# Kernel tuning notes

Hardware: AMD Instinct MI355X
Metric: run time of the kernel (lower is better)

Reference implementation:

```python
import jax, jax.numpy as jnp
import numpy as np
from jax import lax

N = 8192          # number of proposals
CLASSES = 81      # includes background class 0
PAD = 300         # padding (max detections kept)
NMS_THRESH = 0.5


def _decode_and_pick(metadata, deltas, proposals, scores):
    """bbox_transform_inv + clip + per-row argmax class gather (keras_rcnn math)."""
    scale = metadata[0, 2]
    boxes = proposals.reshape(-1, 4) / scale                      # (N,4) x1,y1,x2,y2
    n = boxes.shape[0]
    d = deltas.reshape(n, -1, 4)                                  # (N,C,4) dx,dy,dw,dh
    s = scores.reshape(n, -1)                                     # (N,C)

    w = boxes[:, 2] - boxes[:, 0] + 1.0
    h = boxes[:, 3] - boxes[:, 1] + 1.0
    cx = boxes[:, 0] + 0.5 * w
    cy = boxes[:, 1] + 0.5 * h

    pcx = d[:, :, 0] * w[:, None] + cx[:, None]
    pcy = d[:, :, 1] * h[:, None] + cy[:, None]
    pw = jnp.exp(d[:, :, 2]) * w[:, None]
    ph = jnp.exp(d[:, :, 3]) * h[:, None]

    pred = jnp.stack([pcx - 0.5 * pw, pcy - 0.5 * ph,
                      pcx + 0.5 * pw, pcy + 0.5 * ph], axis=-1)   # (N,C,4)

    # clip to image: x cols to [0, W-1], y cols to [0, H-1]; metadata[0,:2]=(H,W)
    H, W = metadata[0, 0], metadata[0, 1]
    lim = jnp.stack([W - 1.0, H - 1.0, W - 1.0, H - 1.0])
    pred = jnp.clip(pred, 0.0, lim)

    top = jnp.argmax(s, axis=1)                                   # (N,)
    sel = jnp.take_along_axis(pred, top[:, None, None], axis=1)[:, 0, :]  # (N,4)
    max_scores = jnp.max(s[:, 1:], axis=1)                        # exclude background
    return sel, s, max_scores


def _nms_indices(boxes, scores):
    """Greedy NMS; returns (PAD,) kept indices + float validity mask."""
    n = boxes.shape[0]
    order = jnp.argsort(-scores)
    b = boxes[order]
    x1, y1, x2, y2 = b[:, 0], b[:, 1], b[:, 2], b[:, 3]
    area = jnp.maximum(x2 - x1, 0.0) * jnp.maximum(y2 - y1, 0.0)
    lt = jnp.maximum(b[:, None, :2], b[None, :, :2])
    rb = jnp.minimum(b[:, None, 2:], b[None, :, 2:])
    wh = jnp.maximum(rb - lt, 0.0)
    inter = wh[..., 0] * wh[..., 1]                               # (N,N)
    iou = inter / (area[:, None] + area[None, :] - inter + 1e-8)

    idx = jnp.arange(n)

    def step(suppressed, xs):
        iou_row, i = xs
        keep_i = jnp.logical_not(suppressed[i])
        suppressed = suppressed | (keep_i & (iou_row > NMS_THRESH) & (idx > i))
        return suppressed, keep_i

    _, keep = lax.scan(step, jnp.zeros((n,), bool), (iou, idx))    # keep in sorted order

    rank = jnp.cumsum(keep.astype(jnp.int32)) - 1
    pos = jnp.where(keep & (rank < PAD), rank, PAD)               # overflow slot PAD
    buf = jnp.zeros((PAD + 1,), jnp.int32).at[pos].set(order.astype(jnp.int32))
    keep_idx = buf[:PAD]
    num_kept = jnp.minimum(jnp.sum(keep.astype(jnp.int32)), PAD)
    valid = (jnp.arange(PAD) < num_kept).astype(boxes.dtype)
    return keep_idx, valid


def setup_inputs() -> dict:
    key = jax.random.key(0)
    k1, k2, k3, k4, k5, k6 = jax.random.split(key, 6)
    Himg, Wimg, scale = 800.0, 1333.0, 1.5
    metadata = jnp.array([[Himg, Wimg, scale]], dtype=jnp.float32)
    cx = jax.random.uniform(k1, (1, N), minval=0.0, maxval=Wimg * scale)
    cy = jax.random.uniform(k2, (1, N), minval=0.0, maxval=Himg * scale)
    w = jax.random.uniform(k3, (1, N), minval=16.0, maxval=256.0)
    h = jax.random.uniform(k4, (1, N), minval=16.0, maxval=256.0)
    proposals = jnp.stack([cx - 0.5 * w, cy - 0.5 * h,
                           cx + 0.5 * w, cy + 0.5 * h], axis=-1)  # (1,N,4)
    deltas = 0.1 * jax.random.normal(k5, (1, N, 4 * CLASSES), dtype=jnp.float32)
    scores = jax.random.uniform(k6, (1, N, CLASSES), dtype=jnp.float32)
    return {"metadata": metadata, "deltas": deltas,
            "proposals": proposals, "scores": scores}


def reference(metadata, deltas, proposals, scores):
    sel, s, max_scores = _decode_and_pick(metadata, deltas, proposals, scores)
    keep_idx, valid = _nms_indices(lax.stop_gradient(sel),
                                   lax.stop_gradient(max_scores))
    boxes_out = sel[keep_idx] * valid[:, None]                    # (PAD,4), zero-padded
    scores_out = s[keep_idx] * valid[:, None]                     # (PAD,C)
    return boxes_out[None], scores_out[None]
```

## Files before the change

kernel.cpp:

```cpp
#include <hip/hip_runtime.h>

#define N 8192
#define NCLS 81
#define PAD 300
#define NPANEL 16
#define PANW 512

typedef unsigned long long u64;

__device__ __forceinline__ void gload_lds16(const void* g, void* l) {
  __builtin_amdgcn_global_load_lds(
      (const __attribute__((address_space(1))) unsigned int*)g,
      (__attribute__((address_space(3))) unsigned int*)l, 16, 0, 0);
}

__device__ __forceinline__ u64 readlane64(u64 v, int l) {
  unsigned lo = __builtin_amdgcn_readlane((unsigned)v, l);
  unsigned hi = __builtin_amdgcn_readlane((unsigned)(v >> 32), l);
  return ((u64)hi << 32) | lo;
}

__global__ __launch_bounds__(256) void decode_kernel(
    const float* __restrict__ meta, const float* __restrict__ deltas,
    const float* __restrict__ proposals, const float* __restrict__ scores,
    float4* __restrict__ sel, u64* __restrict__ keys, int* __restrict__ rank,
    int* __restrict__ ctr) {
  int tid = threadIdx.x;
  if (blockIdx.x == 0 && tid < 16) ctr[tid] = 0;
  int row = blockIdx.x * 32 + (tid >> 3);
  int sub = tid & 7;
  const float* srow = scores + (size_t)row * NCLS;
  float bs = -1e30f, ms = -1e30f;
  int best = 0;
  for (int c = sub; c < NCLS; c += 8) {
    float v = srow[c];
    if (v > bs) { bs = v; best = c; }
    if (c > 0) ms = fmaxf(ms, v);
  }
#pragma unroll
  for (int d = 1; d < 8; d <<= 1) {
    float ob = __shfl_xor(bs, d);
    int oi = __shfl_xor(best, d);
    float om = __shfl_xor(ms, d);
    if (ob > bs || (ob == bs && oi < best)) { bs = ob; best = oi; }
    ms = fmaxf(ms, om);
  }
  if (sub == 0) {
    float W = meta[1], sc = meta[2], H = meta[0];
    const float* p = proposals + row * 4;
    float x1 = p[0] / sc, y1 = p[1] / sc, x2 = p[2] / sc, y2 = p[3] / sc;
    float w = x2 - x1 + 1.0f, h = y2 - y1 + 1.0f;
    float cx = x1 + 0.5f * w, cy = y1 + 0.5f * h;
    float4 d4 = *(const float4*)(deltas + (size_t)row * (4 * NCLS) + best * 4);
    float pcx = d4.x * w + cx, pcy = d4.y * h + cy;
    float pw = expf(d4.z) * w, ph = expf(d4.w) * h;
    float lx = W - 1.0f, ly = H - 1.0f;
    float ox1 = fminf(fmaxf(pcx - 0.5f * pw, 0.0f), lx);
    float oy1 = fminf(fmaxf(pcy - 0.5f * ph, 0.0f), ly);
    float ox2 = fminf(fmaxf(pcx + 0.5f * pw, 0.0f), lx);
    float oy2 = fminf(fmaxf(pcy + 0.5f * ph, 0.0f), ly);
    sel[row] = make_float4(ox1, oy1, ox2, oy2);
    keys[row] = ((u64)(~__float_as_uint(ms)) << 32) | (unsigned)row;
    rank[row] = 0;
  }
}

__global__ __launch_bounds__(256) void rank_kernel(
    const u64* __restrict__ keys, int* __restrict__ rank) {
  __shared__ u64 kt[256];
  int tid = threadIdx.x;
  int i = blockIdx.x * 256 + tid;
  kt[tid] = keys[blockIdx.y * 256 + tid];
  u64 ki = keys[i];
  __syncthreads();
  int c = 0;
#pragma unroll 8
  for (int t = 0; t < 256; ++t) c += (kt[t] < ki);
  atomicAdd(&rank[i], c);
}

__global__ __launch_bounds__(256) void scatter_kernel(
    const int* __restrict__ rank, const float4* __restrict__ sel,
    int* __restrict__ sortedIdx, float4* __restrict__ sortedBoxes,
    float* __restrict__ sortedArea) {
  int i = blockIdx.x * 256 + threadIdx.x;
  int r = rank[i];
  float4 b = sel[i];
  sortedIdx[r] = i;
  sortedBoxes[r] = b;
  sortedArea[r] = fmaxf(b.z - b.x, 0.0f) * fmaxf(b.w - b.y, 0.0f);
}

__global__ __launch_bounds__(256) void mask_scan_kernel(
    const float4* __restrict__ sboxes, const float* __restrict__ sarea,
    u64* __restrict__ mask, int* __restrict__ kept, int* __restrict__ num_kept,
    int* __restrict__ ctr) {
  __shared__ union {
    u64 slab[PANW * 8];
    struct { float4 cbox[256]; float carea[256]; } m;
  } sh;
  __shared__ int keptGi[PAD];
  int tid = threadIdx.x;

  if (blockIdx.x > 0) {
    int idx = (int)blockIdx.x - 1;
    int cb = idx >> 5, rg = idx & 31;
    if (4 * rg > cb) return;
    int rbase = rg * 256;
    sh.m.cbox[tid] = sboxes[rbase + tid];
    sh.m.carea[tid] = sarea[rbase + tid];
    int lane = tid & 63, wid = tid >> 6;
    float4 bj = sboxes[cb * 64 + lane];
    float aB = sarea[cb * 64 + lane];
    __syncthreads();
    int rlim = cb * 64 + 64;
    int r0 = rbase + (wid << 6);
#pragma unroll 4
    for (int i = 0; i < 32; ++i) {
      int r1 = r0 + i, r2 = r0 + i + 32;
      if (r1 >= rlim) break;
      float4 bi1 = sh.m.cbox[(wid << 6) + i];
      float aA1 = sh.m.carea[(wid << 6) + i];
      float4 bi2 = sh.m.cbox[(wid << 6) + i + 32];
      float aA2 = sh.m.carea[(wid << 6) + i + 32];
      float lx1 = fmaxf(bi1.x, bj.x), ly1 = fmaxf(bi1.y, bj.y);
      float rx1 = fminf(bi1.z, bj.z), ry1 = fminf(bi1.w, bj.w);
      float in1 = fmaxf(rx1 - lx1, 0.0f) * fmaxf(ry1 - ly1, 0.0f);
      float u1 = aA1 + aB - in1 + 1e-8f;
      u64 bits1 = __ballot(((in1 * 33554432.0f - u1 * 16777216.0f) - u1) > 0.0f);
      float lx2 = fmaxf(bi2.x, bj.x), ly2 = fmaxf(bi2.y, bj.y);
      float rx2 = fminf(bi2.z, bj.z), ry2 = fminf(bi2.w, bj.w);
      float in2 = fmaxf(rx2 - lx2, 0.0f) * fmaxf(ry2 - ly2, 0.0f);
      float u2 = aA2 + aB - in2 + 1e-8f;
      u64 bits2 = __ballot(((in2 * 33554432.0f - u2 * 16777216.0f) - u2) > 0.0f);
      if ((r1 >> 6) == cb) bits1 &= ~((2ull << (r1 & 63)) - 1ull);
      if ((r2 >> 6) == cb) bits2 &= ~((2ull << (r2 & 63)) - 1ull);
      if (lane == 0) {
        __hip_atomic_store(&mask[(size_t)r1 * 128 + cb], bits1,
                           __ATOMIC_RELAXED, __HIP_MEMORY_SCOPE_AGENT);
        if (r2 < rlim)
          __hip_atomic_store(&mask[(size_t)r2 * 128 + cb], bits2,
                             __ATOMIC_RELAXED, __HIP_MEMORY_SCOPE_AGENT);
      }
    }
    __syncthreads();
    if (tid == 0)
      __hip_atomic_fetch_add(&ctr[cb >> 3], 1, __ATOMIC_RELEASE,
                             __HIP_MEMORY_SCOPE_AGENT);
    return;
  }

  if (tid >= 64) return;
  int lane = tid;
  int cnt = 0;
  const char* mb = (const char*)mask;

  for (int p = 0; p < NPANEL; ++p) {
    int base = p * PANW;
    int need = 16 * p + 12;
    while (__hip_atomic_load(&ctr[p], __ATOMIC_RELAXED,
                             __HIP_MEMORY_SCOPE_AGENT) < need)
      __builtin_amdgcn_s_sleep(8);
    (void)__hip_atomic_load(&ctr[p], __ATOMIC_ACQUIRE,
                            __HIP_MEMORY_SCOPE_AGENT);

    {
      const char* srcB = mb + (size_t)base * 1024 + (size_t)p * 64;
#pragma unroll
      for (int it = 0; it < 32; ++it) {
        const char* g = srcB + (size_t)(it * 16 + (lane >> 2)) * 1024 + (lane & 3) * 16;
        gload_lds16(g, &sh.slab[0] + it * 128);
      }
    }
    u64 d0 = mask[(size_t)(base + 0 + lane) * 128 + p * 8 + 0];
    u64 d1 = mask[(size_t)(base + 64 + lane) * 128 + p * 8 + 1];
    u64 d2 = mask[(size_t)(base + 128 + lane) * 128 + p * 8 + 2];
    u64 d3 = mask[(size_t)(base + 192 + lane) * 128 + p * 8 + 3];
    u64 d4 = mask[(size_t)(base + 256 + lane) * 128 + p * 8 + 4];
    u64 d5 = mask[(size_t)(base + 320 + lane) * 128 + p * 8 + 5];
    u64 d6 = mask[(size_t)(base + 384 + lane) * 128 + p * 8 + 6];
    u64 d7 = mask[(size_t)(base + 448 + lane) * 128 + p * 8 + 7];
    u64 acc = 0ull;
    for (int k = (lane >> 3); k < cnt; k += 8)
      acc |= mask[(size_t)keptGi[k] * 128 + p * 8 + (lane & 7)];

    asm volatile("s_waitcnt vmcnt(0)" ::: "memory");
    __builtin_amdgcn_sched_barrier(0);

    acc |= __shfl_xor(acc, 8);
    acc |= __shfl_xor(acc, 16);
    acc |= __shfl_xor(acc, 32);
    u64 remv = acc;
    const u64* sl = sh.slab;

    unsigned wm = (unsigned)__ballot(~remv != 0ull) & 0xFFu;
    while (cnt < PAD && wm) {
      int w = __ffs(wm) - 1;
      u64 diagW = (w == 0) ? d0 : (w == 1) ? d1 : (w == 2) ? d2 : (w == 3) ? d3
                : (w == 4) ? d4 : (w == 5) ? d5 : (w == 6) ? d6 : d7;
      u64 cur = __shfl(remv, w);
      u64 kb = 0ull;
      while (true) {
        u64 inv = ~cur;
        if (inv == 0ull) break;
        int b = __ffsll(inv) - 1;
        u64 mrow = readlane64(diagW, b);
        if (lane == 0) kept[cnt] = base + (w << 6) + b;
        keptGi[cnt] = base + (w << 6) + b;
        cnt++;
        kb |= 1ull << b;
        cur |= mrow | (1ull << b);
        if (cnt >= PAD) break;
      }
      u64 t = kb;
      while (t) {
        int b = __ffsll(t) - 1;
        t &= t - 1;
        remv |= sl[((w << 6) + b) * 8 + (lane & 7)];
      }
      if ((lane & 7) == w) remv |= kb;
      if (cnt >= PAD) break;
      wm = (unsigned)__ballot(~remv != 0ull) & 0xFFu;
    }
    if (cnt >= PAD) break;
  }
  asm volatile("s_waitcnt vmcnt(0)" ::: "memory");
  if (lane == 0) *num_kept = cnt;
}

__global__ __launch_bounds__(128) void gather_kernel(
    const int* __restrict__ kept, const int* __restrict__ num_kept_p,
    const int* __restrict__ sortedIdx, const float4* __restrict__ sortedBoxes,
    const float* __restrict__ scores, float* __restrict__ out) {
  int r = blockIdx.x;
  int t = threadIdx.x;
  float* boxes_out = out;
  float* scores_out = out + PAD * 4;
  int nk = *num_kept_p;
  bool valid = r < nk;
  int pos = valid ? kept[r] : 0;
  if (t < NCLS) {
    int orig = sortedIdx[pos];
    scores_out[(size_t)r * NCLS + t] = valid ? scores[(size_t)orig * NCLS + t] : 0.0f;
  }
  if (t == 96) {
    float4 b = sortedBoxes[pos];
    if (!valid) b = make_float4(0.f, 0.f, 0.f, 0.f);
    ((float4*)boxes_out)[r] = b;
  }
}

extern "C" void kernel_launch(void* const* d_in, const int* in_sizes, int n_in,
                              void* d_out, int out_size, void* d_ws, size_t ws_size,
                              hipStream_t stream) {
  const float* meta = (const float*)d_in[0];
  const float* deltas = (const float*)d_in[1];
  const float* proposals = (const float*)d_in[2];
  const float* scores = (const float*)d_in[3];
  float* out = (float*)d_out;
  char* ws = (char*)d_ws;

  float4* sel = (float4*)(ws + 0);
  u64* keys = (u64*)(ws + 131072);
  int* rank = (int*)(ws + 196608);
  int* sortedIdx = (int*)(ws + 229376);
  float4* sortedBoxes = (float4*)(ws + 262144);
  float* sortedArea = (float*)(ws + 393216);
  int* kept = (int*)(ws + 425984);
  int* num_kept = (int*)(ws + 428032);
  int* ctr = (int*)(ws + 428096);
  u64* mask = (u64*)(ws + 458752);

  decode_kernel<<<N / 32, 256, 0, stream>>>(meta, deltas, proposals, scores, sel, keys, rank, ctr);
  rank_kernel<<<dim3(N / 256, N / 256), 256, 0, stream>>>(keys, rank);
  scatter_kernel<<<N / 256, 256, 0, stream>>>(rank, sel, sortedIdx, sortedBoxes, sortedArea);
  mask_scan_kernel<<<1 + 128 * 32, 256, 0, stream>>>(sortedBoxes, sortedArea, mask, kept, num_kept, ctr);
  gather_kernel<<<PAD, 128, 0, stream>>>(kept, num_kept, sortedIdx, sortedBoxes, scores, out);
}
```

Measured before the change: 88.70 us.

## Double-buffer NMS mask slabs with a producer wave prefetching panels

```diff
diff --git a/kernel.cpp b/kernel.cpp
--- a/kernel.cpp
+++ b/kernel.cpp
@@ -96,10 +96,12 @@
     u64* __restrict__ mask, int* __restrict__ kept, int* __restrict__ num_kept,
     int* __restrict__ ctr) {
   __shared__ union {
-    u64 slab[PANW * 8];
+    u64 slab[2][PANW * 8];
     struct { float4 cbox[256]; float carea[256]; } m;
   } sh;
   __shared__ int keptGi[PAD];
+  __shared__ volatile int slabReady[2];
+  __shared__ volatile int scanPos;
   int tid = threadIdx.x;
 
   if (blockIdx.x > 0) {
@@ -150,28 +152,49 @@
     return;
   }
 
-  if (tid >= 64) return;
-  int lane = tid;
-  int cnt = 0;
-  const char* mb = (const char*)mask;
-
-  for (int p = 0; p < NPANEL; ++p) {
-    int base = p * PANW;
-    int need = 16 * p + 12;
-    while (__hip_atomic_load(&ctr[p], __ATOMIC_RELAXED,
-                             __HIP_MEMORY_SCOPE_AGENT) < need)
-      __builtin_amdgcn_s_sleep(8);
-    (void)__hip_atomic_load(&ctr[p], __ATOMIC_ACQUIRE,
-                            __HIP_MEMORY_SCOPE_AGENT);
-
-    {
-      const char* srcB = mb + (size_t)base * 1024 + (size_t)p * 64;
+  if (tid == 0) { slabReady[0] = -1; slabReady[1] = -1; scanPos = -1; }
+  __syncthreads();
+  if (tid >= 128) return;
+
+  if (tid >= 64) {
+    int lane = tid & 63;
+    for (int p = 0; p < NPANEL; ++p) {
+      int b = p & 1;
+      while (scanPos < p - 2) {
+        if (scanPos >= 90) return;
+        __builtin_amdgcn_s_sleep(2);
+      }
+      if (scanPos >= 90) return;
+      int need = 16 * p + 12;
+      while (__hip_atomic_load(&ctr[p], __ATOMIC_RELAXED,
+                               __HIP_MEMORY_SCOPE_AGENT) < need) {
+        if (scanPos >= 90) return;
+        __builtin_amdgcn_s_sleep(8);
+      }
+      (void)__hip_atomic_load(&ctr[p], __ATOMIC_ACQUIRE,
+                              __HIP_MEMORY_SCOPE_AGENT);
+      const char* srcB = (const char*)mask + (size_t)(p * PANW) * 1024 + (size_t)p * 64;
 #pragma unroll
       for (int it = 0; it < 32; ++it) {
         const char* g = srcB + (size_t)(it * 16 + (lane >> 2)) * 1024 + (lane & 3) * 16;
-        gload_lds16(g, &sh.slab[0] + it * 128);
-      }
+        gload_lds16(g, &sh.slab[b][0] + it * 128);
+      }
+      asm volatile("s_waitcnt vmcnt(0)" ::: "memory");
+      if (lane == 0) slabReady[b] = p;
     }
+    return;
+  }
+
+  int lane = tid;
+  int cnt = 0;
+
+  for (int p = 0; p < NPANEL; ++p) {
+    int b = p & 1;
+    while (slabReady[b] != p) __builtin_amdgcn_s_sleep(2);
+    (void)__hip_atomic_load(&ctr[p], __ATOMIC_ACQUIRE,
+                            __HIP_MEMORY_SCOPE_AGENT);
+    int base = p * PANW;
+
     u64 d0 = mask[(size_t)(base + 0 + lane) * 128 + p * 8 + 0];
     u64 d1 = mask[(size_t)(base + 64 + lane) * 128 + p * 8 + 1];
     u64 d2 = mask[(size_t)(base + 128 + lane) * 128 + p * 8 + 2];
@@ -191,7 +214,7 @@
     acc |= __shfl_xor(acc, 16);
     acc |= __shfl_xor(acc, 32);
     u64 remv = acc;
-    const u64* sl = sh.slab;
+    const u64* sl = &sh.slab[b][0];
 
     unsigned wm = (unsigned)__ballot(~remv != 0ull) & 0xFFu;
     while (cnt < PAD && wm) {
@@ -203,28 +226,29 @@
       while (true) {
         u64 inv = ~cur;
         if (inv == 0ull) break;
-        int b = __ffsll(inv) - 1;
-        u64 mrow = readlane64(diagW, b);
-        if (lane == 0) kept[cnt] = base + (w << 6) + b;
-        keptGi[cnt] = base + (w << 6) + b;
+        int bq = __ffsll(inv) - 1;
+        u64 mrow = readlane64(diagW, bq);
+        if (lane == 0) kept[cnt] = base + (w << 6) + bq;
+        keptGi[cnt] = base + (w << 6) + bq;
         cnt++;
-        kb |= 1ull << b;
-        cur |= mrow | (1ull << b);
+        kb |= 1ull << bq;
+        cur |= mrow | (1ull << bq);
         if (cnt >= PAD) break;
       }
       u64 t = kb;
       while (t) {
-        int b = __ffsll(t) - 1;
+        int bq = __ffsll(t) - 1;
         t &= t - 1;
-        remv |= sl[((w << 6) + b) * 8 + (lane & 7)];
+        remv |= sl[((w << 6) + bq) * 8 + (lane & 7)];
       }
       if ((lane & 7) == w) remv |= kb;
       if (cnt >= PAD) break;
       wm = (unsigned)__ballot(~remv != 0ull) & 0xFFu;
     }
+    if (lane == 0) scanPos = p;
     if (cnt >= PAD) break;
   }
-  asm volatile("s_waitcnt vmcnt(0)" ::: "memory");
+  if (lane == 0) scanPos = 99;
   if (lane == 0) *num_kept = cnt;
 }
 
```

Measured after the change: 96.34 us. +8.6%, slower.
